# Kernel tuning notes

Measured on AMD Instinct MI355X. Metric: run time of the kernel, lower is better.

Reference implementation:

```python
import jax, jax.numpy as jnp
import numpy as np

N, E, C, F = 20000, 320000, 64, 8
DIN = 2 * C + F + 1           # MLP input: sender scalars + receiver scalars + radial feats + length
AVG = 16.0                    # avg_num_neighbors
INV_SQRT3 = 0.5773502691896258


def setup_inputs() -> dict:
    key = jax.random.key(0)
    ks = jax.random.split(key, 16)
    d = {}
    d["node_feats"] = jax.random.normal(ks[0], (N, C + 3 * C), jnp.float32)  # 64x0e + 64x1o (mul-major)
    d["edge_attrs"] = jax.random.normal(ks[1], (E, 4), jnp.float32)           # SH: 1x0e + 1x1o
    d["edge_feats"] = jax.random.normal(ks[2], (E, F), jnp.float32)           # radial basis
    d["lengths"] = jax.random.uniform(ks[3], (E, 1), jnp.float32)
    d["edge_index"] = jax.random.randint(ks[4], (2, E), 0, N, jnp.int32)      # (sender, receiver)
    d["Wsc"] = jax.random.normal(ks[5], (C, C), jnp.float32) / np.sqrt(C).astype(np.float32)
    d["Wup0"] = jax.random.normal(ks[6], (C, C), jnp.float32) / np.sqrt(C).astype(np.float32)
    d["Wup1"] = jax.random.normal(ks[7], (C, C), jnp.float32) / np.sqrt(C).astype(np.float32)
    d["W1"] = jax.random.normal(ks[8], (DIN, C), jnp.float32) / np.sqrt(DIN).astype(np.float32)
    d["b1"] = jnp.zeros((C,), jnp.float32)
    d["W2"] = jax.random.normal(ks[9], (C, C), jnp.float32) / np.sqrt(C).astype(np.float32)
    d["b2"] = jnp.zeros((C,), jnp.float32)
    d["W3"] = jax.random.normal(ks[10], (C, 4 * C), jnp.float32) * 1e-3       # near-zero init like the source
    d["Ws"] = jax.random.normal(ks[11], (2 * C, C), jnp.float32) / np.sqrt(2 * C).astype(np.float32)
    d["Wv"] = jax.random.normal(ks[12], (2 * C, C), jnp.float32) / np.sqrt(2 * C).astype(np.float32)
    return d


def reference(node_feats, edge_attrs, edge_feats, lengths, edge_index,
              Wsc, Wup0, Wup1, W1, b1, W2, b2, W3, Ws, Wv):
    n = node_feats.shape[0]
    s = node_feats[:, :C]                          # [N,C] scalar (0e) channels
    v = node_feats[:, C:].reshape(n, C, 3)         # [N,C,3] vector (1o) channels

    node_scalars = s @ Wsc                          # linear_scalar -> 64x0e
    s_up = s @ Wup0                                 # linear_up, 0e block
    v_up = jnp.einsum('nci,cd->ndi', v, Wup1)       # linear_up, 1o block

    snd, rcv = edge_index[0], edge_index[1]

    # weight MLP: Dense->silu->Dense->silu->Dense(no bias)
    mlp_in = jnp.concatenate([node_scalars[snd], node_scalars[rcv], edge_feats, lengths], axis=-1)
    h = jax.nn.silu(mlp_in @ W1 + b1)
    h = jax.nn.silu(h @ W2 + b2)
    tw = h @ W3                                     # [E, 4C] per-irrep tp weights
    w0, w1, w2, w3 = jnp.split(tw, 4, axis=-1)

    y0 = edge_attrs[:, :1]                          # [E,1] SH l=0
    y1 = edge_attrs[:, 1:4]                         # [E,3] SH l=1
    xs = s_up[snd]                                  # [E,C]   gather senders
    xv = v_up[snd]                                  # [E,C,3]

    # weighted tensor product paths (component normalization), filtered to 0e/1o
    p0 = xs * y0 * w0                                               # 0e x 0e -> 0e  [E,C]
    p1 = (jnp.einsum('eci,ei->ec', xv, y1) * INV_SQRT3) * w1        # 1o x 1o -> 0e  [E,C]
    p2 = xs[:, :, None] * y1[:, None, :] * w2[:, :, None]           # 0e x 1o -> 1o  [E,C,3]
    p3 = xv * y0[:, :, None] * w3[:, :, None]                       # 1o x 0e -> 1o  [E,C,3]

    # scatter_sum messages into receiver nodes
    m0 = jax.ops.segment_sum(jnp.concatenate([p0, p1], axis=-1), rcv, num_segments=n)  # [N,2C]
    m1 = jax.ops.segment_sum(jnp.concatenate([p2, p3], axis=1), rcv, num_segments=n)   # [N,2C,3]

    # final equivariant linear on simplified irreps_mid (128x0e + 128x1o), / avg_num_neighbors
    out_s = (m0 @ Ws) / AVG                          # [N,C]
    out_v = jnp.einsum('nci,cd->ndi', m1, Wv) / AVG  # [N,C,3]

    # reshape_irreps -> [N, channels, 1 + 3]
    return jnp.concatenate([out_s[:, :, None], out_v], axis=-1)
```

## Files before the change

kernel.cpp:

```cpp
#include <hip/hip_runtime.h>

#define N_NODES 20000
#define N_EDGES 320000
#define INV_SQRT3 0.5773502691896258f

typedef unsigned short u16;
typedef unsigned int u32;
typedef __attribute__((ext_vector_type(8))) short short8;
typedef __attribute__((ext_vector_type(8))) _Float16 half8;
typedef __attribute__((ext_vector_type(2))) __fp16 fp16x2;
typedef __attribute__((ext_vector_type(4))) float f32x4;
typedef __attribute__((ext_vector_type(4))) u32 u32x4v;

static const size_t OFF_NSBF = 0;
static const size_t OFF_SV   = 2560000;
static const size_t OFF_MG   = 23040000;
static const size_t OFF_TW   = 64000000;
static const size_t OFF_W1F  = 227840000;
static const size_t OFF_W2F  = 227860480;
static const size_t OFF_W3F  = 227868672;
static const size_t OFF_WNF  = 227901440;
static const size_t OFF_CNT  = 227950592;
static const size_t OFF_OFFS = 228030592;
static const size_t OFF_CUR  = 228110608;
static const size_t OFF_ES   = 228190608;
static const size_t OFF_SS   = 229470608;
static const size_t OFF_RS   = 230750608;
static const size_t OFF_EA   = 232030608;

static __device__ __forceinline__ u16 f2bf(float x) {
    union { float f; u32 u; } c; c.f = x;
    u32 u = c.u + 0x7fffu + ((c.u >> 16) & 1u);
    return (u16)(u >> 16);
}
static __device__ __forceinline__ float bf2f(u16 b) {
    union { u32 u; float f; } c; c.u = (u32)b << 16; return c.f;
}
static __device__ __forceinline__ u16 f2h(float x) {
    union { _Float16 h; u16 u; } c; c.h = (_Float16)x; return c.u;
}
static __device__ __forceinline__ float h2f(u32 b) {
    union { u16 u; _Float16 h; } c; c.u = (u16)b; return (float)c.h;
}
static __device__ __forceinline__ u32 pkh(float a, float b) {
    union { fp16x2 h; u32 u; } c;
    c.h = __builtin_amdgcn_cvt_pkrtz(a, b);
    return c.u;
}
static __device__ __forceinline__ f32x4 mfma16(short8 a, short8 b, f32x4 c) {
    return __builtin_amdgcn_mfma_f32_16x16x32_bf16(a, b, c, 0, 0, 0);
}
static __device__ __forceinline__ f32x4 mfma16h(half8 a, half8 b, f32x4 c) {
    return __builtin_amdgcn_mfma_f32_16x16x32_f16(a, b, c, 0, 0, 0);
}
static __device__ __forceinline__ float silu(float x) {
    return x / (1.0f + __expf(-x));
}
template <typename T>
static __device__ __forceinline__ T ntload(const T* p) { return __builtin_nontemporal_load(p); }
template <typename T>
static __device__ __forceinline__ void ntstore(T* p, T v) { __builtin_nontemporal_store(v, p); }

__global__ void prep_w_kernel(const float* __restrict__ W1, const float* __restrict__ W2,
                              const float* __restrict__ W3,
                              u16* __restrict__ W1f, u16* __restrict__ W2f, u16* __restrict__ W3f) {
    int t = blockIdx.x * 256 + threadIdx.x;
    if (t >= 3840) return;
    int l = t & 63, grp = t >> 6;
    int hi = l >> 4, lo = l & 15;
    if (grp < 20) {
        int kk = grp >> 2, jt = grp & 3;
#pragma unroll
        for (int e2 = 0; e2 < 8; e2++) {
            int k = kk * 32 + hi * 8 + e2, j = jt * 16 + lo;
            W1f[(size_t)(grp * 64 + l) * 8 + e2] = (k < 137) ? f2bf(W1[k * 64 + j]) : (u16)0;
        }
    } else if (grp < 28) {
        int g = grp - 20; int kk = g >> 2, jt = g & 3;
#pragma unroll
        for (int e2 = 0; e2 < 8; e2++) {
            int k = kk * 32 + hi * 8 + e2, j = jt * 16 + lo;
            int kp = ((k & 3) << 4) + (k >> 2);
            W2f[(size_t)(g * 64 + l) * 8 + e2] = f2h(W2[kp * 64 + j]);
        }
    } else {
        int g = grp - 28; int kk = g >> 4, jt = g & 15;
#pragma unroll
        for (int e2 = 0; e2 < 8; e2++) {
            int k = kk * 32 + hi * 8 + e2, j = jt * 16 + lo;
            int kp = ((k & 3) << 4) + (k >> 2);
            W3f[(size_t)(g * 64 + l) * 8 + e2] = f2h(W3[kp * 256 + j]);
        }
    }
}

__global__ void prep_wn_kernel(const float* __restrict__ Wsc, const float* __restrict__ Wup0,
                               const float* __restrict__ Wup1, u16* __restrict__ WNF) {
    int t = blockIdx.x * 256 + threadIdx.x;
    if (t >= 1536) return;
    int mat = t >> 9;
    int rem = t & 511;
    int g = rem >> 6, l = rem & 63;
    int kk = g >> 2, jt = g & 3, hi = l >> 4, lo = l & 15;
    const float* W = (mat == 0) ? Wsc : (mat == 1) ? Wup0 : Wup1;
    u16* dh = WNF + (size_t)mat * 8192 + (size_t)(g * 64 + l) * 8;
    u16* dl = dh + 4096;
#pragma unroll
    for (int e2 = 0; e2 < 8; e2++) {
        int k = kk * 32 + hi * 8 + e2, d = jt * 16 + lo;
        float w = W[k * 64 + d];
        u16 h = f2bf(w);
        dh[e2] = h;
        dl[e2] = f2bf(w - bf2f(h));
    }
}

__global__ void prep_w2_kernel(const float* __restrict__ Ws, const float* __restrict__ Wv,
                               u16* __restrict__ WSF) {
    int t = blockIdx.x * 256 + threadIdx.x;
    if (t >= 2048) return;
    int l = t & 63, grp = t >> 6;
    int wsel = grp >> 4;
    int g = grp & 15;
    int kk = g >> 2, jt = g & 3;
    int hi = l >> 4, lo = l & 15;
    const float* W = wsel ? Wv : Ws;
    u16* dh = WSF + (size_t)wsel * 16384;
    u16* dl = dh + 8192;
    size_t base = (size_t)(g * 64 + l) * 8;
#pragma unroll
    for (int e2 = 0; e2 < 8; e2++) {
        int k = kk * 32 + hi * 8 + e2, d = jt * 16 + lo;
        float w = W[k * 64 + d];
        u16 h = f2bf(w);
        float r = w - bf2f(h);
        dh[base + e2] = h;
        dl[base + e2] = f2bf(r);
    }
}

__global__ __launch_bounds__(256) void node_prep_kernel(
    const float* __restrict__ node_feats, const u16* __restrict__ WNF,
    u16* __restrict__ ns_bf, u16* __restrict__ svh) {
    const int tid = threadIdx.x;
    const int lane = tid & 63;
    const int w = tid >> 6;
    const int lo16 = lane & 15;
    const int hi = lane >> 4;
    const int nb = blockIdx.x * 64 + w * 16;

    int an = nb + lo16; if (an > N_NODES - 1) an = N_NODES - 1;
    const float* arow = node_feats + (size_t)an * 256;

    const short8* B = (const short8*)WNF;

    f32x4 acc_ns[4], acc_su[4], acc_v[3][4];
#pragma unroll
    for (int jt = 0; jt < 4; jt++) {
        acc_ns[jt] = (f32x4)(0.0f);
        acc_su[jt] = (f32x4)(0.0f);
#pragma unroll
        for (int i = 0; i < 3; i++) acc_v[i][jt] = (f32x4)(0.0f);
    }

#pragma unroll
    for (int kk = 0; kk < 2; kk++) {
        short8 sh, sl;
        {
            const float* sp = arow + kk * 32 + hi * 8;
            f32x4 x0 = *(const f32x4*)sp;
            f32x4 x1 = *(const f32x4*)(sp + 4);
#pragma unroll
            for (int j = 0; j < 4; j++) {
                u16 h0 = f2bf(x0[j]);
                sh[j] = (short)h0;
                sl[j] = (short)f2bf(x0[j] - bf2f(h0));
                u16 h1 = f2bf(x1[j]);
                sh[4 + j] = (short)h1;
                sl[4 + j] = (short)f2bf(x1[j] - bf2f(h1));
            }
        }
        short8 vh[3], vl[3];
#pragma unroll
        for (int i = 0; i < 3; i++) {
            const float* vp = arow + 64 + i + 3 * (kk * 32 + hi * 8);
#pragma unroll
            for (int e = 0; e < 8; e++) {
                float x = vp[e * 3];
                u16 hb = f2bf(x);
                vh[i][e] = (short)hb;
                vl[i][e] = (short)f2bf(x - bf2f(hb));
            }
        }
#pragma unroll
        for (int jt = 0; jt < 4; jt++) {
            int fi = (kk * 4 + jt) * 64 + lane;
            short8 bh = B[fi], bl = B[512 + fi];
            acc_ns[jt] = mfma16(sh, bh, acc_ns[jt]);
            acc_ns[jt] = mfma16(sl, bh, acc_ns[jt]);
            acc_ns[jt] = mfma16(sh, bl, acc_ns[jt]);
            bh = B[1024 + fi]; bl = B[1536 + fi];
            acc_su[jt] = mfma16(sh, bh, acc_su[jt]);
            acc_su[jt] = mfma16(sl, bh, acc_su[jt]);
            acc_su[jt] = mfma16(sh, bl, acc_su[jt]);
            bh = B[2048 + fi]; bl = B[2560 + fi];
#pragma unroll
            for (int i = 0; i < 3; i++) {
                acc_v[i][jt] = mfma16(vh[i], bh, acc_v[i][jt]);
                acc_v[i][jt] = mfma16(vl[i], bh, acc_v[i][jt]);
                acc_v[i][jt] = mfma16(vh[i], bl, acc_v[i][jt]);
            }
        }
    }

#pragma unroll
    for (int r = 0; r < 4; r++) {
        int n = nb + hi * 4 + r;
        if (n < N_NODES) {
#pragma unroll
            for (int jt = 0; jt < 4; jt++) {
                int d = jt * 16 + lo16;
                ns_bf[(size_t)n * 64 + d] = f2bf(acc_ns[jt][r]);
                uint2 o;
                o.x = pkh(acc_su[jt][r], acc_v[0][jt][r]);
                o.y = pkh(acc_v[1][jt][r], acc_v[2][jt][r]);
                *(uint2*)&svh[((size_t)n * 64 + d) * 4] = o;
            }
        }
    }
}

__global__ void hist_kernel(const int* __restrict__ ei, int* __restrict__ cnt) {
    int e = blockIdx.x * 256 + threadIdx.x;
    if (e < N_EDGES) atomicAdd(&cnt[ei[N_EDGES + e]], 1);
}

__global__ void scan_kernel(const int* __restrict__ cnt, int* __restrict__ offs,
                            int* __restrict__ cursor) {
    __shared__ int buf[1024];
    int t = threadIdx.x;
    int base = t * 20;
    int loc[20];
    int tot = 0;
    int v20[20];
    if (base < N_NODES) {
#pragma unroll
        for (int q = 0; q < 5; q++) {
            int4 vv = *(const int4*)&cnt[base + q * 4];
            v20[q * 4 + 0] = vv.x; v20[q * 4 + 1] = vv.y;
            v20[q * 4 + 2] = vv.z; v20[q * 4 + 3] = vv.w;
        }
    } else {
#pragma unroll
        for (int i = 0; i < 20; i++) v20[i] = 0;
    }
#pragma unroll
    for (int i = 0; i < 20; i++) { loc[i] = tot; tot += v20[i]; }
    buf[t] = tot;
    __syncthreads();
    for (int d = 1; d < 1024; d <<= 1) {
        int add = (t >= d) ? buf[t - d] : 0;
        __syncthreads();
        buf[t] += add;
        __syncthreads();
    }
    int ebase = buf[t] - tot;
#pragma unroll
    for (int i = 0; i < 20; i++) {
        int idx = base + i;
        if (idx < N_NODES) { int o = ebase + loc[i]; offs[idx] = o; cursor[idx] = o; }
    }
    if (t == 1023) offs[N_NODES] = buf[1023];
}

__global__ void scatter_kernel(const int* __restrict__ ei, const float* __restrict__ edge_attrs,
                               int* __restrict__ cursor,
                               int* __restrict__ esort, int* __restrict__ ssort,
                               int* __restrict__ rsort, float* __restrict__ easort) {
    int e = blockIdx.x * 256 + threadIdx.x;
    if (e < N_EDGES) {
        int sn = ei[e];
        int rc = ei[N_EDGES + e];
        float4 ea = *(const float4*)(edge_attrs + (size_t)e * 4);
        int pos = atomicAdd(&cursor[rc], 1);
        esort[pos] = e;
        ssort[pos] = sn;
        rsort[pos] = rc;
        *(float4*)(easort + (size_t)pos * 4) = ea;
    }
}

__global__ __launch_bounds__(256, 5) void mlp_kernel(
    const u16* __restrict__ ns_bf,
    const u16* __restrict__ W1f, const u16* __restrict__ W2f, const u16* __restrict__ W3f,
    const float* __restrict__ b1, const float* __restrict__ b2,
    const float* __restrict__ edge_feats, const float* __restrict__ lengths,
    const int* __restrict__ esort, const int* __restrict__ ssort, const int* __restrict__ rsort,
    u16* __restrict__ twg) {

    __shared__ u16 mlpbuf[64][168];
    __shared__ u16 h1s[64][72];
    u16* h2sf = &mlpbuf[0][0];

    const int tid = threadIdx.x;
    const int l = tid & 63;
    const int lo16 = l & 15;
    const int hi = l >> 4;
    const int w = tid >> 6;
    const int erow = (w << 4) | lo16;
    const int koff = hi * 8;
    const int drow = (w << 4) + hi * 4;

    const int p0 = blockIdx.x * 64;

    const short8* w1frag = (const short8*)W1f;
    const half8* w2frag = (const half8*)W2f;
    const half8* w3frag = (const half8*)W3f;

    float bb1[4], bb2[4];
#pragma unroll
    for (int jt = 0; jt < 4; jt++) { bb1[jt] = b1[jt * 16 + lo16]; bb2[jt] = b2[jt * 16 + lo16]; }

    {
        int rr = tid >> 2, pp = tid & 3;
        uint4 z = {0, 0, 0, 0};
        *(uint4*)&mlpbuf[rr][136 + pp * 8] = z;
    }

    {
        int es = tid >> 2, part = tid & 3;
        int e = esort[p0 + es];
        int sn = ssort[p0 + es];
        int rc = rsort[p0 + es];
        const uint4* ps = (const uint4*)(ns_bf + (size_t)sn * 64 + part * 16);
        uint4 s0 = ps[0], s1 = ps[1];
        *(uint4*)&mlpbuf[es][part * 16] = s0;
        *(uint4*)&mlpbuf[es][part * 16 + 8] = s1;
        const uint4* pr = (const uint4*)(ns_bf + (size_t)rc * 64 + part * 16);
        uint4 r0v = pr[0], r1v = pr[1];
        *(uint4*)&mlpbuf[es][64 + part * 16] = r0v;
        *(uint4*)&mlpbuf[es][64 + part * 16 + 8] = r1v;
        if (part == 0) {
            float4 f0 = *(const float4*)(edge_feats + (size_t)e * 8);
            float4 f1 = *(const float4*)(edge_feats + (size_t)e * 8 + 4);
            u32 pk0 = (u32)f2bf(f0.x) | ((u32)f2bf(f0.y) << 16);
            u32 pk1 = (u32)f2bf(f0.z) | ((u32)f2bf(f0.w) << 16);
            u32 pk2 = (u32)f2bf(f1.x) | ((u32)f2bf(f1.y) << 16);
            u32 pk3 = (u32)f2bf(f1.z) | ((u32)f2bf(f1.w) << 16);
            uint4 pk = {pk0, pk1, pk2, pk3};
            *(uint4*)&mlpbuf[es][128] = pk;
            mlpbuf[es][136] = f2bf(lengths[e]);
        }
    }
    __syncthreads();

    f32x4 a1c[4];
#pragma unroll
    for (int jt = 0; jt < 4; jt++) a1c[jt] = (f32x4)(0.0f);
#pragma unroll
    for (int kk = 0; kk < 5; kk++) {
        short8 af = *(const short8*)&mlpbuf[erow][kk * 32 + koff];
        const short8* wb = w1frag + kk * 256 + l;
        a1c[0] = mfma16(af, wb[0],   a1c[0]);
        a1c[1] = mfma16(af, wb[64],  a1c[1]);
        a1c[2] = mfma16(af, wb[128], a1c[2]);
        a1c[3] = mfma16(af, wb[192], a1c[3]);
    }
#pragma unroll
    for (int r = 0; r < 4; r++) {
        uint2 pk;
        pk.x = pkh(silu(a1c[0][r] + bb1[0]), silu(a1c[1][r] + bb1[1]));
        pk.y = pkh(silu(a1c[2][r] + bb1[2]), silu(a1c[3][r] + bb1[3]));
        *(uint2*)&h1s[drow + r][lo16 * 4] = pk;
    }
    __syncthreads();

    f32x4 a2c[4];
#pragma unroll
    for (int jt = 0; jt < 4; jt++) a2c[jt] = (f32x4)(0.0f);
#pragma unroll
    for (int kk = 0; kk < 2; kk++) {
        half8 af = *(const half8*)&h1s[erow][kk * 32 + koff];
        const half8* wb = w2frag + kk * 256 + l;
        a2c[0] = mfma16h(af, wb[0],   a2c[0]);
        a2c[1] = mfma16h(af, wb[64],  a2c[1]);
        a2c[2] = mfma16h(af, wb[128], a2c[2]);
        a2c[3] = mfma16h(af, wb[192], a2c[3]);
    }
#pragma unroll
    for (int r = 0; r < 4; r++) {
        uint2 pk;
        pk.x = pkh(silu(a2c[0][r] + bb2[0]), silu(a2c[1][r] + bb2[1]));
        pk.y = pkh(silu(a2c[2][r] + bb2[2]), silu(a2c[3][r] + bb2[3]));
        *(uint2*)&h2sf[(drow + r) * 72 + lo16 * 4] = pk;
    }
    __syncthreads();

    f32x4 tw[16];
#pragma unroll
    for (int jt = 0; jt < 16; jt++) tw[jt] = (f32x4)(0.0f);
#pragma unroll
    for (int kk = 0; kk < 2; kk++) {
        half8 af = *(const half8*)&h2sf[erow * 72 + kk * 32 + koff];
        const half8* wb = w3frag + kk * 1024 + l;
#pragma unroll
        for (int jt = 0; jt < 16; jt++) tw[jt] = mfma16h(af, wb[jt * 64], tw[jt]);
    }

    int relrow = p0 + drow;
#pragma unroll
    for (int r = 0; r < 4; r++) {
        u32x4v A, B;
        A.x = pkh(tw[0][r],  tw[1][r]);
        A.y = pkh(tw[2][r],  tw[3][r]);
        A.z = pkh(tw[4][r],  tw[5][r]);
        A.w = pkh(tw[6][r],  tw[7][r]);
        B.x = pkh(tw[8][r],  tw[9][r]);
        B.y = pkh(tw[10][r], tw[11][r]);
        B.z = pkh(tw[12][r], tw[13][r]);
        B.w = pkh(tw[14][r], tw[15][r]);
        u16* dst = twg + (size_t)(relrow + r) * 256 + lo16 * 16;
        *(u32x4v*)dst = A;
        *(((u32x4v*)dst) + 1) = B;
    }
}

__global__ __launch_bounds__(256, 4) void seg_kernel(
    const u16* __restrict__ svh, const float* __restrict__ easort,
    const int* __restrict__ ssort,
    const int* __restrict__ offs, const u16* __restrict__ twg,
    float* __restrict__ m_g) {
    const int lane = threadIdx.x & 63;
    const int wv = threadIdx.x >> 6;
    const int n = blockIdx.x * 4 + wv;
    const int c = lane;
    const int jt = c >> 4, lo16 = c & 15;
    const int e0 = offs[n], e1 = offs[n + 1];
    float a_m0 = 0.f, a_m0b = 0.f;
    float a20 = 0.f, a21 = 0.f, a22 = 0.f, a30 = 0.f, a31 = 0.f, a32 = 0.f;
#pragma unroll 4
    for (int pos = e0; pos < e1; ++pos) {
        int sn = ssort[pos];
        const u16* twp = twg + (size_t)pos * 256 + lo16 * 16;
        u32x4v ta = *((const u32x4v*)twp);
        u32x4v tb = *(((const u32x4v*)twp) + 1);
        f32x4 y4 = *(const f32x4*)(easort + (size_t)pos * 4);
        uint2 sp = *(const uint2*)&svh[((size_t)sn * 64 + c) * 4];
        u32 wwa = (jt & 2) ? ta.y : ta.x;
        u32 wwb = (jt & 2) ? ta.w : ta.z;
        u32 wwc = (jt & 2) ? tb.y : tb.x;
        u32 wwd = (jt & 2) ? tb.w : tb.z;
        int sh = (jt & 1) << 4;
        float w0 = h2f((wwa >> sh) & 0xffffu);
        float w1 = h2f((wwb >> sh) & 0xffffu);
        float w2 = h2f((wwc >> sh) & 0xffffu);
        float w3 = h2f((wwd >> sh) & 0xffffu);
        float xs  = h2f(sp.x & 0xffffu);
        float xv0 = h2f(sp.x >> 16);
        float xv1 = h2f(sp.y & 0xffffu);
        float xv2 = h2f(sp.y >> 16);
        float y0 = y4.x, ya = y4.y, yb = y4.z, yc = y4.w;
        a_m0 = fmaf(xs * y0, w0, a_m0);
        float dv = xv0 * ya + xv1 * yb + xv2 * yc;
        a_m0b = fmaf(dv, w1, a_m0b);
        float sw2 = xs * w2;
        a20 = fmaf(sw2, ya, a20); a21 = fmaf(sw2, yb, a21); a22 = fmaf(sw2, yc, a22);
        float yw3 = y0 * w3;
        a30 = fmaf(xv0, yw3, a30); a31 = fmaf(xv1, yw3, a31); a32 = fmaf(xv2, yw3, a32);
    }
    float* mr = m_g + (size_t)n * 512;
    ntstore(mr + c,        a_m0);
    ntstore(mr + 64 + c,   a_m0b * INV_SQRT3);
    ntstore(mr + 128 + c,  a20);
    ntstore(mr + 192 + c,  a30);
    ntstore(mr + 256 + c,  a21);
    ntstore(mr + 320 + c,  a31);
    ntstore(mr + 384 + c,  a22);
    ntstore(mr + 448 + c,  a32);
}

__global__ __launch_bounds__(256, 2) void out_kernel(
    const float* __restrict__ m_g, const u16* __restrict__ WSF,
    float* __restrict__ out) {
    const int tid = threadIdx.x;
    const int lane = tid & 63;
    const int w = tid >> 6;
    const int lo16 = lane & 15;
    const int hi = lane >> 4;
    const int nb = blockIdx.x * 64 + w * 16;

    int arow_n = nb + lo16;
    if (arow_n > N_NODES - 1) arow_n = N_NODES - 1;
    const float* arow = m_g + (size_t)arow_n * 512 + hi * 8;

    const short8* bsh = (const short8*)WSF;
    const short8* bsl = (const short8*)(WSF + 8192);
    const short8* bvh = (const short8*)(WSF + 16384);
    const short8* bvl = (const short8*)(WSF + 24576);

    f32x4 acc[4][4];
#pragma unroll
    for (int q = 0; q < 4; q++)
#pragma unroll
        for (int jt = 0; jt < 4; jt++) acc[q][jt] = (f32x4)(0.0f);

#pragma unroll
    for (int kk = 0; kk < 4; kk++) {
        short8 ahi[4], alo[4];
#pragma unroll
        for (int q = 0; q < 4; q++) {
            const float* p = arow + q * 128 + kk * 32;
            f32x4 x0 = ntload((const f32x4*)p);
            f32x4 x1 = ntload((const f32x4*)(p + 4));
#pragma unroll
            for (int j = 0; j < 4; j++) {
                u16 h0 = f2bf(x0[j]);
                ahi[q][j] = (short)h0;
                alo[q][j] = (short)f2bf(x0[j] - bf2f(h0));
                u16 h1 = f2bf(x1[j]);
                ahi[q][4 + j] = (short)h1;
                alo[q][4 + j] = (short)f2bf(x1[j] - bf2f(h1));
            }
        }
#pragma unroll
        for (int jt = 0; jt < 4; jt++) {
            int bidx = (kk * 4 + jt) * 64 + lane;
            short8 wh_s = bsh[bidx];
            short8 wl_s = bsl[bidx];
            short8 wh_v = bvh[bidx];
            short8 wl_v = bvl[bidx];
            acc[0][jt] = mfma16(ahi[0], wh_s, acc[0][jt]);
            acc[0][jt] = mfma16(alo[0], wh_s, acc[0][jt]);
            acc[0][jt] = mfma16(ahi[0], wl_s, acc[0][jt]);
#pragma unroll
            for (int q = 1; q < 4; q++) {
                acc[q][jt] = mfma16(ahi[q], wh_v, acc[q][jt]);
                acc[q][jt] = mfma16(alo[q], wh_v, acc[q][jt]);
                acc[q][jt] = mfma16(ahi[q], wl_v, acc[q][jt]);
            }
        }
    }

#pragma unroll
    for (int r = 0; r < 4; r++) {
        int n = nb + hi * 4 + r;
        if (n < N_NODES) {
#pragma unroll
            for (int jt = 0; jt < 4; jt++) {
                int d = jt * 16 + lo16;
                f32x4 o;
                o.x = acc[0][jt][r] * 0.0625f;
                o.y = acc[1][jt][r] * 0.0625f;
                o.z = acc[2][jt][r] * 0.0625f;
                o.w = acc[3][jt][r] * 0.0625f;
                ntstore((f32x4*)(out + (size_t)n * 256 + d * 4), o);
            }
        }
    }
}

extern "C" void kernel_launch(void* const* d_in, const int* in_sizes, int n_in,
                              void* d_out, int out_size, void* d_ws, size_t ws_size,
                              hipStream_t stream) {
    (void)in_sizes; (void)n_in; (void)out_size; (void)ws_size;
    const float* node_feats = (const float*)d_in[0];
    const float* edge_attrs = (const float*)d_in[1];
    const float* edge_feats = (const float*)d_in[2];
    const float* lengths    = (const float*)d_in[3];
    const int*   edge_index = (const int*)d_in[4];
    const float* Wsc  = (const float*)d_in[5];
    const float* Wup0 = (const float*)d_in[6];
    const float* Wup1 = (const float*)d_in[7];
    const float* W1   = (const float*)d_in[8];
    const float* b1   = (const float*)d_in[9];
    const float* W2   = (const float*)d_in[10];
    const float* b2   = (const float*)d_in[11];
    const float* W3   = (const float*)d_in[12];
    const float* Ws   = (const float*)d_in[13];
    const float* Wv   = (const float*)d_in[14];

    char* ws = (char*)d_ws;
    u16*   ns_bf  = (u16*)(ws + OFF_NSBF);
    u16*   svh    = (u16*)(ws + OFF_SV);
    float* m_g    = (float*)(ws + OFF_MG);
    u16*   twg    = (u16*)(ws + OFF_TW);
    u16*   W1f    = (u16*)(ws + OFF_W1F);
    u16*   W2f    = (u16*)(ws + OFF_W2F);
    u16*   W3f    = (u16*)(ws + OFF_W3F);
    u16*   WNF    = (u16*)(ws + OFF_WNF);
    int*   cnt    = (int*)(ws + OFF_CNT);
    int*   offs   = (int*)(ws + OFF_OFFS);
    int*   cursor = (int*)(ws + OFF_CUR);
    u16*   WSF    = (u16*)(ws + OFF_CUR);
    int*   esort  = (int*)(ws + OFF_ES);
    int*   ssort  = (int*)(ws + OFF_SS);
    int*   rsort  = (int*)(ws + OFF_RS);
    float* easort = (float*)(ws + OFF_EA);
    float* out    = (float*)d_out;

    (void)hipMemsetAsync(cnt, 0, N_NODES * sizeof(int), stream);
    prep_w_kernel<<<15, 256, 0, stream>>>(W1, W2, W3, W1f, W2f, W3f);
    prep_wn_kernel<<<6, 256, 0, stream>>>(Wsc, Wup0, Wup1, WNF);
    node_prep_kernel<<<(N_NODES + 63) / 64, 256, 0, stream>>>(node_feats, WNF, ns_bf, svh);
    hist_kernel<<<N_EDGES / 256, 256, 0, stream>>>(edge_index, cnt);
    scan_kernel<<<1, 1024, 0, stream>>>(cnt, offs, cursor);
    scatter_kernel<<<N_EDGES / 256, 256, 0, stream>>>(edge_index, edge_attrs, cursor,
                                                      esort, ssort, rsort, easort);
    prep_w2_kernel<<<8, 256, 0, stream>>>(Ws, Wv, WSF);

    mlp_kernel<<<N_EDGES / 64, 256, 0, stream>>>(ns_bf, W1f, W2f, W3f, b1, b2,
                                                 edge_feats, lengths,
                                                 esort, ssort, rsort, twg);
    seg_kernel<<<N_NODES / 4, 256, 0, stream>>>(svh, easort, ssort,
                                                offs, twg, m_g);
    out_kernel<<<(N_NODES + 63) / 64, 256, 0, stream>>>(m_g, WSF, out);
}
```

Baseline: 247.0 us.

## Presort edge feats in scatter and double-buffer gathers across two MLP tiles

The scatter kernel now converts edge_feats and lengths to bf16 and writes them in receiver-sorted order, so the MLP kernel reads them contiguously instead of through an indirect esort lookup. Each MLP block now handles 128 edges as two 64-edge tiles and issues the global gathers for the second tile before computing the first, hiding gather latency behind MFMA work. This costs more registers to hold the prefetched data, so the launch bound drops from 5 to 4 blocks per SM, and the scatter kernel does extra conversion and writes.

```diff
diff --git a/kernel.cpp b/kernel.cpp
--- a/kernel.cpp
+++ b/kernel.cpp
@@ -23,10 +23,11 @@
 static const size_t OFF_CNT  = 227950592;
 static const size_t OFF_OFFS = 228030592;
 static const size_t OFF_CUR  = 228110608;
-static const size_t OFF_ES   = 228190608;
 static const size_t OFF_SS   = 229470608;
 static const size_t OFF_RS   = 230750608;
 static const size_t OFF_EA   = 232030608;
+static const size_t OFF_EF   = 237150608;
+static const size_t OFF_LEN  = 242270608;
 
 static __device__ __forceinline__ u16 f2bf(float x) {
     union { float f; u32 u; } c; c.f = x;
@@ -274,28 +275,39 @@
 }
 
 __global__ void scatter_kernel(const int* __restrict__ ei, const float* __restrict__ edge_attrs,
+                               const float* __restrict__ edge_feats, const float* __restrict__ lengths,
                                int* __restrict__ cursor,
-                               int* __restrict__ esort, int* __restrict__ ssort,
-                               int* __restrict__ rsort, float* __restrict__ easort) {
+                               int* __restrict__ ssort, int* __restrict__ rsort,
+                               float* __restrict__ easort, u16* __restrict__ efsort,
+                               u16* __restrict__ lsort) {
     int e = blockIdx.x * 256 + threadIdx.x;
     if (e < N_EDGES) {
         int sn = ei[e];
         int rc = ei[N_EDGES + e];
         float4 ea = *(const float4*)(edge_attrs + (size_t)e * 4);
+        float4 f0 = *(const float4*)(edge_feats + (size_t)e * 8);
+        float4 f1 = *(const float4*)(edge_feats + (size_t)e * 8 + 4);
+        float len = lengths[e];
+        uint4 pk;
+        pk.x = (u32)f2bf(f0.x) | ((u32)f2bf(f0.y) << 16);
+        pk.y = (u32)f2bf(f0.z) | ((u32)f2bf(f0.w) << 16);
+        pk.z = (u32)f2bf(f1.x) | ((u32)f2bf(f1.y) << 16);
+        pk.w = (u32)f2bf(f1.z) | ((u32)f2bf(f1.w) << 16);
         int pos = atomicAdd(&cursor[rc], 1);
-        esort[pos] = e;
         ssort[pos] = sn;
         rsort[pos] = rc;
         *(float4*)(easort + (size_t)pos * 4) = ea;
-    }
-}
-
-__global__ __launch_bounds__(256, 5) void mlp_kernel(
+        *(uint4*)(efsort + (size_t)pos * 8) = pk;
+        lsort[pos] = f2bf(len);
+    }
+}
+
+__global__ __launch_bounds__(256, 4) void mlp_kernel(
     const u16* __restrict__ ns_bf,
     const u16* __restrict__ W1f, const u16* __restrict__ W2f, const u16* __restrict__ W3f,
     const float* __restrict__ b1, const float* __restrict__ b2,
-    const float* __restrict__ edge_feats, const float* __restrict__ lengths,
-    const int* __restrict__ esort, const int* __restrict__ ssort, const int* __restrict__ rsort,
+    const int* __restrict__ ssort, const int* __restrict__ rsort,
+    const u16* __restrict__ efsort, const u16* __restrict__ lsort,
     u16* __restrict__ twg) {
 
     __shared__ u16 mlpbuf[64][168];
@@ -310,8 +322,7 @@
     const int erow = (w << 4) | lo16;
     const int koff = hi * 8;
     const int drow = (w << 4) + hi * 4;
-
-    const int p0 = blockIdx.x * 64;
+    const int es = tid >> 2, part = tid & 3;
 
     const short8* w1frag = (const short8*)W1f;
     const half8* w2frag = (const half8*)W2f;
@@ -321,108 +332,122 @@
 #pragma unroll
     for (int jt = 0; jt < 4; jt++) { bb1[jt] = b1[jt * 16 + lo16]; bb2[jt] = b2[jt * 16 + lo16]; }
 
-    {
-        int rr = tid >> 2, pp = tid & 3;
-        uint4 z = {0, 0, 0, 0};
-        *(uint4*)&mlpbuf[rr][136 + pp * 8] = z;
-    }
-
-    {
-        int es = tid >> 2, part = tid & 3;
-        int e = esort[p0 + es];
-        int sn = ssort[p0 + es];
-        int rc = rsort[p0 + es];
-        const uint4* ps = (const uint4*)(ns_bf + (size_t)sn * 64 + part * 16);
-        uint4 s0 = ps[0], s1 = ps[1];
-        *(uint4*)&mlpbuf[es][part * 16] = s0;
-        *(uint4*)&mlpbuf[es][part * 16 + 8] = s1;
-        const uint4* pr = (const uint4*)(ns_bf + (size_t)rc * 64 + part * 16);
-        uint4 r0v = pr[0], r1v = pr[1];
-        *(uint4*)&mlpbuf[es][64 + part * 16] = r0v;
-        *(uint4*)&mlpbuf[es][64 + part * 16 + 8] = r1v;
-        if (part == 0) {
-            float4 f0 = *(const float4*)(edge_feats + (size_t)e * 8);
-            float4 f1 = *(const float4*)(edge_feats + (size_t)e * 8 + 4);
-            u32 pk0 = (u32)f2bf(f0.x) | ((u32)f2bf(f0.y) << 16);
-            u32 pk1 = (u32)f2bf(f0.z) | ((u32)f2bf(f0.w) << 16);
-            u32 pk2 = (u32)f2bf(f1.x) | ((u32)f2bf(f1.y) << 16);
-            u32 pk3 = (u32)f2bf(f1.z) | ((u32)f2bf(f1.w) << 16);
-            uint4 pk = {pk0, pk1, pk2, pk3};
-            *(uint4*)&mlpbuf[es][128] = pk;
-            mlpbuf[es][136] = f2bf(lengths[e]);
-        }
-    }
+    const int p0 = blockIdx.x * 128;
+
+    uint4 g_s0, g_s1, g_r0, g_r1, g_ef;
+    u16 g_len = 0;
+
+#define GATHER(P)                                                              \
+    {                                                                          \
+        int sn_ = ssort[(P) + es];                                             \
+        int rc_ = rsort[(P) + es];                                             \
+        const uint4* ps_ = (const uint4*)(ns_bf + (size_t)sn_ * 64 + part * 16); \
+        g_s0 = ps_[0]; g_s1 = ps_[1];                                          \
+        const uint4* pr_ = (const uint4*)(ns_bf + (size_t)rc_ * 64 + part * 16); \
+        g_r0 = pr_[0]; g_r1 = pr_[1];                                          \
+        if (part == 0) {                                                       \
+            g_ef = *(const uint4*)(efsort + (size_t)((P) + es) * 8);           \
+            g_len = lsort[(P) + es];                                           \
+        }                                                                      \
+    }
+
+#define STAGE()                                                                \
+    {                                                                          \
+        *(uint4*)&mlpbuf[es][part * 16] = g_s0;                                \
+        *(uint4*)&mlpbuf[es][part * 16 + 8] = g_s1;                            \
+        *(uint4*)&mlpbuf[es][64 + part * 16] = g_r0;                           \
+        *(uint4*)&mlpbuf[es][64 + part * 16 + 8] = g_r1;                       \
+        uint4 z_ = {0, 0, 0, 0};                                               \
+        *(uint4*)&mlpbuf[es][136 + part * 8] = z_;                             \
+        if (part == 0) {                                                       \
+            *(uint4*)&mlpbuf[es][128] = g_ef;                                  \
+            mlpbuf[es][136] = g_len;                                           \
+        }                                                                      \
+    }
+
+#define COMPUTE(P)                                                             \
+    {                                                                          \
+        f32x4 a1c[4];                                                          \
+        _Pragma("unroll")                                                      \
+        for (int jt = 0; jt < 4; jt++) a1c[jt] = (f32x4)(0.0f);                \
+        _Pragma("unroll")                                                      \
+        for (int kk = 0; kk < 5; kk++) {                                       \
+            short8 af = *(const short8*)&mlpbuf[erow][kk * 32 + koff];         \
+            const short8* wb = w1frag + kk * 256 + l;                          \
+            a1c[0] = mfma16(af, wb[0],   a1c[0]);                              \
+            a1c[1] = mfma16(af, wb[64],  a1c[1]);                              \
+            a1c[2] = mfma16(af, wb[128], a1c[2]);                              \
+            a1c[3] = mfma16(af, wb[192], a1c[3]);                              \
+        }                                                                      \
+        _Pragma("unroll")                                                      \
+        for (int r = 0; r < 4; r++) {                                          \
+            uint2 pk;                                                          \
+            pk.x = pkh(silu(a1c[0][r] + bb1[0]), silu(a1c[1][r] + bb1[1]));    \
+            pk.y = pkh(silu(a1c[2][r] + bb1[2]), silu(a1c[3][r] + bb1[3]));    \
+            *(uint2*)&h1s[drow + r][lo16 * 4] = pk;                            \
+        }                                                                      \
+        __syncthreads();                                                       \
+        f32x4 a2c[4];                                                          \
+        _Pragma("unroll")                                                      \
+        for (int jt = 0; jt < 4; jt++) a2c[jt] = (f32x4)(0.0f);                \
+        _Pragma("unroll")                                                      \
+        for (int kk = 0; kk < 2; kk++) {                                       \
+            half8 af = *(const half8*)&h1s[erow][kk * 32 + koff];              \
+            const half8* wb = w2frag + kk * 256 + l;                           \
+            a2c[0] = mfma16h(af, wb[0],   a2c[0]);                             \
+            a2c[1] = mfma16h(af, wb[64],  a2c[1]);                             \
+            a2c[2] = mfma16h(af, wb[128], a2c[2]);                             \
+            a2c[3] = mfma16h(af, wb[192], a2c[3]);                             \
+        }                                                                      \
+        _Pragma("unroll")                                                      \
+        for (int r = 0; r < 4; r++) {                                          \
+            uint2 pk;                                                          \
+            pk.x = pkh(silu(a2c[0][r] + bb2[0]), silu(a2c[1][r] + bb2[1]));    \
+            pk.y = pkh(silu(a2c[2][r] + bb2[2]), silu(a2c[3][r] + bb2[3]));    \
+            *(uint2*)&h2sf[(drow + r) * 72 + lo16 * 4] = pk;                   \
+        }                                                                      \
+        __syncthreads();                                                       \
+        f32x4 tw[16];                                                          \
+        _Pragma("unroll")                                                      \
+        for (int jt = 0; jt < 16; jt++) tw[jt] = (f32x4)(0.0f);                \
+        _Pragma("unroll")                                                      \
+        for (int kk = 0; kk < 2; kk++) {                                       \
+            half8 af = *(const half8*)&h2sf[erow * 72 + kk * 32 + koff];       \
+            const half8* wb = w3frag + kk * 1024 + l;                          \
+            _Pragma("unroll")                                                  \
+            for (int jt = 0; jt < 16; jt++) tw[jt] = mfma16h(af, wb[jt * 64], tw[jt]); \
+        }                                                                      \
+        int relrow = (P) + drow;                                               \
+        _Pragma("unroll")                                                      \
+        for (int r = 0; r < 4; r++) {                                          \
+            u32x4v A, B;                                                       \
+            A.x = pkh(tw[0][r],  tw[1][r]);                                    \
+            A.y = pkh(tw[2][r],  tw[3][r]);                                    \
+            A.z = pkh(tw[4][r],  tw[5][r]);                                    \
+            A.w = pkh(tw[6][r],  tw[7][r]);                                    \
+            B.x = pkh(tw[8][r],  tw[9][r]);                                    \
+            B.y = pkh(tw[10][r], tw[11][r]);                                   \
+            B.z = pkh(tw[12][r], tw[13][r]);                                   \
+            B.w = pkh(tw[14][r], tw[15][r]);                                   \
+            u16* dst = twg + (size_t)(relrow + r) * 256 + lo16 * 16;           \
+            *(u32x4v*)dst = A;                                                 \
+            *(((u32x4v*)dst) + 1) = B;                                         \
+        }                                                                      \
+    }
+
+    GATHER(p0);
+    STAGE();
     __syncthreads();
-
-    f32x4 a1c[4];
-#pragma unroll
-    for (int jt = 0; jt < 4; jt++) a1c[jt] = (f32x4)(0.0f);
-#pragma unroll
-    for (int kk = 0; kk < 5; kk++) {
-        short8 af = *(const short8*)&mlpbuf[erow][kk * 32 + koff];
-        const short8* wb = w1frag + kk * 256 + l;
-        a1c[0] = mfma16(af, wb[0],   a1c[0]);
-        a1c[1] = mfma16(af, wb[64],  a1c[1]);
-        a1c[2] = mfma16(af, wb[128], a1c[2]);
-        a1c[3] = mfma16(af, wb[192], a1c[3]);
-    }
-#pragma unroll
-    for (int r = 0; r < 4; r++) {
-        uint2 pk;
-        pk.x = pkh(silu(a1c[0][r] + bb1[0]), silu(a1c[1][r] + bb1[1]));
-        pk.y = pkh(silu(a1c[2][r] + bb1[2]), silu(a1c[3][r] + bb1[3]));
-        *(uint2*)&h1s[drow + r][lo16 * 4] = pk;
-    }
+    GATHER(p0 + 64);
+    COMPUTE(p0);
     __syncthreads();
-
-    f32x4 a2c[4];
-#pragma unroll
-    for (int jt = 0; jt < 4; jt++) a2c[jt] = (f32x4)(0.0f);
-#pragma unroll
-    for (int kk = 0; kk < 2; kk++) {
-        half8 af = *(const half8*)&h1s[erow][kk * 32 + koff];
-        const half8* wb = w2frag + kk * 256 + l;
-        a2c[0] = mfma16h(af, wb[0],   a2c[0]);
-        a2c[1] = mfma16h(af, wb[64],  a2c[1]);
-        a2c[2] = mfma16h(af, wb[128], a2c[2]);
-        a2c[3] = mfma16h(af, wb[192], a2c[3]);
-    }
-#pragma unroll
-    for (int r = 0; r < 4; r++) {
-        uint2 pk;
-        pk.x = pkh(silu(a2c[0][r] + bb2[0]), silu(a2c[1][r] + bb2[1]));
-        pk.y = pkh(silu(a2c[2][r] + bb2[2]), silu(a2c[3][r] + bb2[3]));
-        *(uint2*)&h2sf[(drow + r) * 72 + lo16 * 4] = pk;
-    }
+    STAGE();
     __syncthreads();
-
-    f32x4 tw[16];
-#pragma unroll
-    for (int jt = 0; jt < 16; jt++) tw[jt] = (f32x4)(0.0f);
-#pragma unroll
-    for (int kk = 0; kk < 2; kk++) {
-        half8 af = *(const half8*)&h2sf[erow * 72 + kk * 32 + koff];
-        const half8* wb = w3frag + kk * 1024 + l;
-#pragma unroll
-        for (int jt = 0; jt < 16; jt++) tw[jt] = mfma16h(af, wb[jt * 64], tw[jt]);
-    }
-
-    int relrow = p0 + drow;
-#pragma unroll
-    for (int r = 0; r < 4; r++) {
-        u32x4v A, B;
-        A.x = pkh(tw[0][r],  tw[1][r]);
-        A.y = pkh(tw[2][r],  tw[3][r]);
-        A.z = pkh(tw[4][r],  tw[5][r]);
-        A.w = pkh(tw[6][r],  tw[7][r]);
-        B.x = pkh(tw[8][r],  tw[9][r]);
-        B.y = pkh(tw[10][r], tw[11][r]);
-        B.z = pkh(tw[12][r], tw[13][r]);
-        B.w = pkh(tw[14][r], tw[15][r]);
-        u16* dst = twg + (size_t)(relrow + r) * 256 + lo16 * 16;
-        *(u32x4v*)dst = A;
-        *(((u32x4v*)dst) + 1) = B;
-    }
+    COMPUTE(p0 + 64);
+
+#undef GATHER
+#undef STAGE
+#undef COMPUTE
 }
 
 __global__ __launch_bounds__(256, 4) void seg_kernel(
@@ -592,10 +617,11 @@
     int*   offs   = (int*)(ws + OFF_OFFS);
     int*   cursor = (int*)(ws + OFF_CUR);
     u16*   WSF    = (u16*)(ws + OFF_CUR);
-    int*   esort  = (int*)(ws + OFF_ES);
     int*   ssort  = (int*)(ws + OFF_SS);
     int*   rsort  = (int*)(ws + OFF_RS);
     float* easort = (float*)(ws + OFF_EA);
+    u16*   efsort = (u16*)(ws + OFF_EF);
+    u16*   lsort  = (u16*)(ws + OFF_LEN);
     float* out    = (float*)d_out;
 
     (void)hipMemsetAsync(cnt, 0, N_NODES * sizeof(int), stream);
@@ -604,13 +630,13 @@
     node_prep_kernel<<<(N_NODES + 63) / 64, 256, 0, stream>>>(node_feats, WNF, ns_bf, svh);
     hist_kernel<<<N_EDGES / 256, 256, 0, stream>>>(edge_index, cnt);
     scan_kernel<<<1, 1024, 0, stream>>>(cnt, offs, cursor);
-    scatter_kernel<<<N_EDGES / 256, 256, 0, stream>>>(edge_index, edge_attrs, cursor,
-                                                      esort, ssort, rsort, easort);
+    scatter_kernel<<<N_EDGES / 256, 256, 0, stream>>>(edge_index, edge_attrs, edge_feats,
+                                                      lengths, cursor,
+                                                      ssort, rsort, easort, efsort, lsort);
     prep_w2_kernel<<<8, 256, 0, stream>>>(Ws, Wv, WSF);
 
-    mlp_kernel<<<N_EDGES / 64, 256, 0, stream>>>(ns_bf, W1f, W2f, W3f, b1, b2,
-                                                 edge_feats, lengths,
-                                                 esort, ssort, rsort, twg);
+    mlp_kernel<<<N_EDGES / 128, 256, 0, stream>>>(ns_bf, W1f, W2f, W3f, b1, b2,
+                                                  ssort, rsort, efsort, lsort, twg);
     seg_kernel<<<N_NODES / 4, 256, 0, stream>>>(svh, easort, ssort,
                                                 offs, twg, m_g);
     out_kernel<<<(N_NODES + 63) / 64, 256, 0, stream>>>(m_g, WSF, out);
```

Result: slower. 282.3 us (+14.3%).

## Pre-sort edge feats in scatter and relayout MLP weights for per-channel reads

Applied to the files above, without the earlier changes.

The scatter kernel now converts edge_feats and lengths to bf16 and writes them in receiver-sorted order, so the MLP kernel reads them contiguously instead of gathering through an edge permutation. This also drops the esort array. The MLP output is re-laid out so each channel's four path weights sit in one 8-byte group, letting seg_kernel load them with one uint2 instead of two 16-byte loads plus lane selects. The cost is extra scattered writes in the scatter kernel and more but smaller stores in the MLP epilogue.

```diff
diff --git a/kernel.cpp b/kernel.cpp
--- a/kernel.cpp
+++ b/kernel.cpp
@@ -23,10 +23,11 @@
 static const size_t OFF_CNT  = 227950592;
 static const size_t OFF_OFFS = 228030592;
 static const size_t OFF_CUR  = 228110608;
-static const size_t OFF_ES   = 228190608;
 static const size_t OFF_SS   = 229470608;
 static const size_t OFF_RS   = 230750608;
 static const size_t OFF_EA   = 232030608;
+static const size_t OFF_EF   = 237150608;
+static const size_t OFF_LEN  = 242270608;
 
 static __device__ __forceinline__ u16 f2bf(float x) {
     union { float f; u32 u; } c; c.f = x;
@@ -274,19 +275,30 @@
 }
 
 __global__ void scatter_kernel(const int* __restrict__ ei, const float* __restrict__ edge_attrs,
+                               const float* __restrict__ edge_feats, const float* __restrict__ lengths,
                                int* __restrict__ cursor,
-                               int* __restrict__ esort, int* __restrict__ ssort,
-                               int* __restrict__ rsort, float* __restrict__ easort) {
+                               int* __restrict__ ssort, int* __restrict__ rsort,
+                               float* __restrict__ easort, u16* __restrict__ efsort,
+                               u16* __restrict__ lsort) {
     int e = blockIdx.x * 256 + threadIdx.x;
     if (e < N_EDGES) {
         int sn = ei[e];
         int rc = ei[N_EDGES + e];
         float4 ea = *(const float4*)(edge_attrs + (size_t)e * 4);
+        float4 f0 = *(const float4*)(edge_feats + (size_t)e * 8);
+        float4 f1 = *(const float4*)(edge_feats + (size_t)e * 8 + 4);
+        float len = lengths[e];
+        uint4 pk;
+        pk.x = (u32)f2bf(f0.x) | ((u32)f2bf(f0.y) << 16);
+        pk.y = (u32)f2bf(f0.z) | ((u32)f2bf(f0.w) << 16);
+        pk.z = (u32)f2bf(f1.x) | ((u32)f2bf(f1.y) << 16);
+        pk.w = (u32)f2bf(f1.z) | ((u32)f2bf(f1.w) << 16);
         int pos = atomicAdd(&cursor[rc], 1);
-        esort[pos] = e;
         ssort[pos] = sn;
         rsort[pos] = rc;
         *(float4*)(easort + (size_t)pos * 4) = ea;
+        *(uint4*)(efsort + (size_t)pos * 8) = pk;
+        lsort[pos] = f2bf(len);
     }
 }
 
@@ -294,8 +306,8 @@
     const u16* __restrict__ ns_bf,
     const u16* __restrict__ W1f, const u16* __restrict__ W2f, const u16* __restrict__ W3f,
     const float* __restrict__ b1, const float* __restrict__ b2,
-    const float* __restrict__ edge_feats, const float* __restrict__ lengths,
-    const int* __restrict__ esort, const int* __restrict__ ssort, const int* __restrict__ rsort,
+    const int* __restrict__ ssort, const int* __restrict__ rsort,
+    const u16* __restrict__ efsort, const u16* __restrict__ lsort,
     u16* __restrict__ twg) {
 
     __shared__ u16 mlpbuf[64][168];
@@ -329,7 +341,6 @@
 
     {
         int es = tid >> 2, part = tid & 3;
-        int e = esort[p0 + es];
         int sn = ssort[p0 + es];
         int rc = rsort[p0 + es];
         const uint4* ps = (const uint4*)(ns_bf + (size_t)sn * 64 + part * 16);
@@ -341,15 +352,9 @@
         *(uint4*)&mlpbuf[es][64 + part * 16] = r0v;
         *(uint4*)&mlpbuf[es][64 + part * 16 + 8] = r1v;
         if (part == 0) {
-            float4 f0 = *(const float4*)(edge_feats + (size_t)e * 8);
-            float4 f1 = *(const float4*)(edge_feats + (size_t)e * 8 + 4);
-            u32 pk0 = (u32)f2bf(f0.x) | ((u32)f2bf(f0.y) << 16);
-            u32 pk1 = (u32)f2bf(f0.z) | ((u32)f2bf(f0.w) << 16);
-            u32 pk2 = (u32)f2bf(f1.x) | ((u32)f2bf(f1.y) << 16);
-            u32 pk3 = (u32)f2bf(f1.z) | ((u32)f2bf(f1.w) << 16);
-            uint4 pk = {pk0, pk1, pk2, pk3};
+            uint4 pk = *(const uint4*)(efsort + (size_t)(p0 + es) * 8);
             *(uint4*)&mlpbuf[es][128] = pk;
-            mlpbuf[es][136] = f2bf(lengths[e]);
+            mlpbuf[es][136] = lsort[p0 + es];
         }
     }
     __syncthreads();
@@ -410,18 +415,14 @@
     int relrow = p0 + drow;
 #pragma unroll
     for (int r = 0; r < 4; r++) {
-        u32x4v A, B;
-        A.x = pkh(tw[0][r],  tw[1][r]);
-        A.y = pkh(tw[2][r],  tw[3][r]);
-        A.z = pkh(tw[4][r],  tw[5][r]);
-        A.w = pkh(tw[6][r],  tw[7][r]);
-        B.x = pkh(tw[8][r],  tw[9][r]);
-        B.y = pkh(tw[10][r], tw[11][r]);
-        B.z = pkh(tw[12][r], tw[13][r]);
-        B.w = pkh(tw[14][r], tw[15][r]);
-        u16* dst = twg + (size_t)(relrow + r) * 256 + lo16 * 16;
-        *(u32x4v*)dst = A;
-        *(((u32x4v*)dst) + 1) = B;
+        u16* dst = twg + (size_t)(relrow + r) * 256 + lo16 * 4;
+#pragma unroll
+        for (int jt4 = 0; jt4 < 4; jt4++) {
+            uint2 pk;
+            pk.x = pkh(tw[jt4][r],     tw[4 + jt4][r]);
+            pk.y = pkh(tw[8 + jt4][r], tw[12 + jt4][r]);
+            *(uint2*)(dst + jt4 * 64) = pk;
+        }
     }
 }
 
@@ -434,27 +435,19 @@
     const int wv = threadIdx.x >> 6;
     const int n = blockIdx.x * 4 + wv;
     const int c = lane;
-    const int jt = c >> 4, lo16 = c & 15;
     const int e0 = offs[n], e1 = offs[n + 1];
     float a_m0 = 0.f, a_m0b = 0.f;
     float a20 = 0.f, a21 = 0.f, a22 = 0.f, a30 = 0.f, a31 = 0.f, a32 = 0.f;
 #pragma unroll 4
     for (int pos = e0; pos < e1; ++pos) {
         int sn = ssort[pos];
-        const u16* twp = twg + (size_t)pos * 256 + lo16 * 16;
-        u32x4v ta = *((const u32x4v*)twp);
-        u32x4v tb = *(((const u32x4v*)twp) + 1);
+        uint2 tq = *(const uint2*)(twg + (size_t)pos * 256 + c * 4);
         f32x4 y4 = *(const f32x4*)(easort + (size_t)pos * 4);
         uint2 sp = *(const uint2*)&svh[((size_t)sn * 64 + c) * 4];
-        u32 wwa = (jt & 2) ? ta.y : ta.x;
-        u32 wwb = (jt & 2) ? ta.w : ta.z;
-        u32 wwc = (jt & 2) ? tb.y : tb.x;
-        u32 wwd = (jt & 2) ? tb.w : tb.z;
-        int sh = (jt & 1) << 4;
-        float w0 = h2f((wwa >> sh) & 0xffffu);
-        float w1 = h2f((wwb >> sh) & 0xffffu);
-        float w2 = h2f((wwc >> sh) & 0xffffu);
-        float w3 = h2f((wwd >> sh) & 0xffffu);
+        float w0 = h2f(tq.x & 0xffffu);
+        float w1 = h2f(tq.x >> 16);
+        float w2 = h2f(tq.y & 0xffffu);
+        float w3 = h2f(tq.y >> 16);
         float xs  = h2f(sp.x & 0xffffu);
         float xv0 = h2f(sp.x >> 16);
         float xv1 = h2f(sp.y & 0xffffu);
@@ -592,10 +585,11 @@
     int*   offs   = (int*)(ws + OFF_OFFS);
     int*   cursor = (int*)(ws + OFF_CUR);
     u16*   WSF    = (u16*)(ws + OFF_CUR);
-    int*   esort  = (int*)(ws + OFF_ES);
     int*   ssort  = (int*)(ws + OFF_SS);
     int*   rsort  = (int*)(ws + OFF_RS);
     float* easort = (float*)(ws + OFF_EA);
+    u16*   efsort = (u16*)(ws + OFF_EF);
+    u16*   lsort  = (u16*)(ws + OFF_LEN);
     float* out    = (float*)d_out;
 
     (void)hipMemsetAsync(cnt, 0, N_NODES * sizeof(int), stream);
@@ -604,13 +598,13 @@
     node_prep_kernel<<<(N_NODES + 63) / 64, 256, 0, stream>>>(node_feats, WNF, ns_bf, svh);
     hist_kernel<<<N_EDGES / 256, 256, 0, stream>>>(edge_index, cnt);
     scan_kernel<<<1, 1024, 0, stream>>>(cnt, offs, cursor);
-    scatter_kernel<<<N_EDGES / 256, 256, 0, stream>>>(edge_index, edge_attrs, cursor,
-                                                      esort, ssort, rsort, easort);
+    scatter_kernel<<<N_EDGES / 256, 256, 0, stream>>>(edge_index, edge_attrs, edge_feats,
+                                                      lengths, cursor,
+                                                      ssort, rsort, easort, efsort, lsort);
     prep_w2_kernel<<<8, 256, 0, stream>>>(Ws, Wv, WSF);
 
     mlp_kernel<<<N_EDGES / 64, 256, 0, stream>>>(ns_bf, W1f, W2f, W3f, b1, b2,
-                                                 edge_feats, lengths,
-                                                 esort, ssort, rsort, twg);
+                                                 ssort, rsort, efsort, lsort, twg);
     seg_kernel<<<N_NODES / 4, 256, 0, stream>>>(svh, easort, ssort,
                                                 offs, twg, m_g);
     out_kernel<<<(N_NODES + 63) / 64, 256, 0, stream>>>(m_g, WSF, out);
```

Measured after the change: 236.5 us. 1.04x faster.
